# Kernel optimization log

Hardware: AMD Instinct MI355X
Metric: run time of the kernel (lower is better)

Reference implementation:

```python
import jax, jax.numpy as jnp
import numpy as np

N = 100_000          # nodes
E = 3_200_000        # train edges (avg degree 32)
E_TEST = 500_000     # pos/neg test edges each
F_IN, F_HID, F_OUT = 256, 16, 64


def setup_inputs() -> dict:
    key = jax.random.key(0)
    ks = jax.random.split(key, 7)
    x = jax.random.normal(ks[0], (N, F_IN), jnp.float32)
    train_edge_index = jax.random.randint(ks[1], (2, E), 0, N, dtype=jnp.int32)
    test_pos_edge_index = jax.random.randint(ks[2], (2, E_TEST), 0, N, dtype=jnp.int32)
    test_neg_edge_index = jax.random.randint(ks[3], (2, E_TEST), 0, N, dtype=jnp.int32)
    W1 = jax.random.normal(ks[4], (F_IN, F_HID), jnp.float32) / np.float32(np.sqrt(F_IN))
    b1 = jnp.zeros((F_HID,), jnp.float32)
    W2 = jax.random.normal(ks[5], (F_HID, F_OUT), jnp.float32) / np.float32(np.sqrt(F_HID))
    b2 = jnp.zeros((F_OUT,), jnp.float32)
    return dict(x=x, train_edge_index=train_edge_index,
                test_pos_edge_index=test_pos_edge_index,
                test_neg_edge_index=test_neg_edge_index,
                W1=W1, b1=b1, W2=W2, b2=b2)


def gcn_conv(x, edge_index, W, b, n):
    """PyG GCNConv: x' = D^-1/2 (A+I) D^-1/2 (x W) + b (self-loops added)."""
    h = x @ W                                  # project first (PyG order)
    loop = jnp.arange(n, dtype=edge_index.dtype)
    src = jnp.concatenate([edge_index[0], loop])
    dst = jnp.concatenate([edge_index[1], loop])
    deg = jax.ops.segment_sum(jnp.ones_like(dst, dtype=h.dtype), dst, num_segments=n)
    dinv = jnp.where(deg > 0, jax.lax.rsqrt(deg), 0.0)
    norm = dinv[src] * dinv[dst]               # per-edge symmetric norm
    msg = h[src] * norm[:, None]               # gather + scale
    out = jax.ops.segment_sum(msg, dst, num_segments=n)  # scatter-add
    return out + b


def reference(x, train_edge_index, test_pos_edge_index, test_neg_edge_index,
              W1, b1, W2, b2):
    n = x.shape[0]
    z = gcn_conv(x, train_edge_index, W1, b1, n)
    z = jax.nn.relu(z)
    z = gcn_conv(z, train_edge_index, W2, b2, n)
    edge_index = jnp.concatenate([test_pos_edge_index, test_neg_edge_index], axis=-1)
    logits = jnp.sum(z[edge_index[0]] * z[edge_index[1]], axis=-1)
    return logits
```

## Files before the change

### kernel.cpp

```cpp
#include <hip/hip_runtime.h>


#define NB_SHIFT 8
#define CAP   9728
#define CHUNK 8192

__global__ void seedprep_kernel(int* __restrict__ gtail, int nb1,
                                const float* __restrict__ W2, const float* __restrict__ b2,
                                float* __restrict__ mw) {
    int t = threadIdx.x;
    for (int i = t; i < nb1; i += 256) gtail[i] = i * CAP;
    int r = t >> 4, cc = t & 15;
    float s = 0.0f;
    for (int j = 0; j < 64; ++j) s += W2[r * 64 + j] * W2[cc * 64 + j];
    mw[t] = s;
    if (t < 16) {
        float w = 0.0f;
        for (int j = 0; j < 64; ++j) w += W2[t * 64 + j] * b2[j];
        mw[256 + t] = w;
    }
    if (t == 0) {
        float bbv = 0.0f;
        for (int j = 0; j < 64; ++j) bbv += b2[j] * b2[j];
        mw[272] = bbv;
    }
}

__global__ void __launch_bounds__(512, 4)
k1_kernel(const int* __restrict__ src, const int* __restrict__ dst, int E,
          int* __restrict__ gtail, unsigned* __restrict__ tmp, int nb1,
          const float* __restrict__ x, const float* __restrict__ W1,
          float* __restrict__ hs, int n, int nblkG) {
    int t = threadIdx.x;
    if ((int)blockIdx.x < nblkG) {
        int row = blockIdx.x * 512 + t;
        if (row >= n) return;
        const float4* x4 = (const float4*)(x + (size_t)row * 256);
        const float4* W14 = (const float4*)W1;
        float4 a0 = {0,0,0,0}, a1 = {0,0,0,0}, a2 = {0,0,0,0}, a3 = {0,0,0,0};
        float4 buf[8];
        #pragma unroll
        for (int j = 0; j < 8; ++j) buf[j] = x4[j];
        for (int k8 = 0; k8 < 8; ++k8) {
            float4 cur[8];
            #pragma unroll
            for (int j = 0; j < 8; ++j) cur[j] = buf[j];
            if (k8 < 7) {
                #pragma unroll
                for (int j = 0; j < 8; ++j) buf[j] = x4[(k8 + 1) * 8 + j];
            }
            #pragma unroll
            for (int jj = 0; jj < 8; ++jj) {
                float4 xv = cur[jj];
                int k4 = k8 * 8 + jj;
                #pragma unroll
                for (int j = 0; j < 4; ++j) {
                    float xk = (j == 0) ? xv.x : (j == 1) ? xv.y : (j == 2) ? xv.z : xv.w;
                    int k = (k4 << 2) + j;
                    float4 w0 = W14[k * 4 + 0];
                    float4 w1 = W14[k * 4 + 1];
                    float4 w2 = W14[k * 4 + 2];
                    float4 w3 = W14[k * 4 + 3];
                    a0.x += xk * w0.x; a0.y += xk * w0.y; a0.z += xk * w0.z; a0.w += xk * w0.w;
                    a1.x += xk * w1.x; a1.y += xk * w1.y; a1.z += xk * w1.z; a1.w += xk * w1.w;
                    a2.x += xk * w2.x; a2.y += xk * w2.y; a2.z += xk * w2.z; a2.w += xk * w2.w;
                    a3.x += xk * w3.x; a3.y += xk * w3.y; a3.z += xk * w3.z; a3.w += xk * w3.w;
                }
            }
        }
        float4* o = (float4*)(hs + (size_t)row * 16);
        o[0] = a0; o[1] = a1; o[2] = a2; o[3] = a3;
        return;
    }

    __shared__ int h[512];
    __shared__ int loff[512];
    __shared__ int cur[512];
    __shared__ int base[512];
    __shared__ unsigned srec[CHUNK];
    __shared__ unsigned short sbkt[CHUNK];
    int c0 = (blockIdx.x - nblkG) * CHUNK;
    int ce = min(CHUNK, E - c0);

    h[t] = 0;
    __syncthreads();
    for (int i = t; i < ce; i += 512)
        atomicAdd(&h[dst[c0 + i] >> NB_SHIFT], 1);
    __syncthreads();
    int cnt = h[t];
    loff[t] = cnt;
    __syncthreads();
    for (int off = 1; off < 512; off <<= 1) {
        int v = loff[t];
        int a = (t >= off) ? loff[t - off] : 0;
        __syncthreads();
        loff[t] = v + a;
        __syncthreads();
    }
    int excl = loff[t] - cnt;
    if (t < nb1) base[t] = atomicAdd(&gtail[t], cnt);
    loff[t] = excl;
    cur[t]  = excl;
    __syncthreads();
    for (int i = t; i < ce; i += 512) {
        int d = dst[c0 + i];
        int s = src[c0 + i];
        int b = d >> NB_SHIFT;
        int p = atomicAdd(&cur[b], 1);
        srec[p] = (unsigned)s | ((unsigned)(d & 255) << 20);
        sbkt[p] = (unsigned short)b;
    }
    __syncthreads();
    for (int i = t; i < ce; i += 512) {
        int b = sbkt[i];
        tmp[base[b] + (i - loff[b])] = srec[i];
    }
}

__global__ void __launch_bounds__(512)
fill2_kernel(const int* __restrict__ gtail, const unsigned* __restrict__ tmp,
             int* __restrict__ eidx, int* __restrict__ rowptr,
             int* __restrict__ counts, float* __restrict__ dinv,
             float* __restrict__ hs, int n) {
    __shared__ int hh[256];
    __shared__ int sc[256];
    __shared__ int cur[256];
    __shared__ float sdinv[256];
    __shared__ int sout[CAP];
    int b = blockIdx.x;
    int t = threadIdx.x;
    int beg = b * CAP;
    int cnt_total = gtail[b] - beg;

    if (t < 256) hh[t] = 0;
    __syncthreads();
    for (int i = t; i < cnt_total; i += 512)
        atomicAdd(&hh[tmp[beg + i] >> 20], 1);
    __syncthreads();
    if (t < 256) sc[t] = hh[t];
    __syncthreads();
    for (int off = 1; off < 256; off <<= 1) {
        int v = 0, a = 0;
        if (t < 256) { v = sc[t]; a = (t >= off) ? sc[t - off] : 0; }
        __syncthreads();
        if (t < 256) sc[t] = v + a;
        __syncthreads();
    }
    if (t < 256) {
        int ex = sc[t] - hh[t];
        cur[t] = ex;
        float dv = rsqrtf((float)hh[t] + 1.0f);
        sdinv[t] = dv;
        int v = (b << NB_SHIFT) + t;
        if (v < n) {
            rowptr[v] = beg + ex;
            counts[v] = hh[t];
            dinv[v]   = dv;
        }
    }
    __syncthreads();
    for (int i = t; i < cnt_total; i += 512) {
        unsigned r = tmp[beg + i];
        int p = atomicAdd(&cur[r >> 20], 1);
        sout[p] = (int)(r & 0xFFFFF);
    }
    __syncthreads();
    for (int i = t; i < cnt_total; i += 512)
        eidx[beg + i] = sout[i];
    int v0 = b << NB_SHIFT;
    int rows = min(256, n - v0);
    if (rows > 0) {
        float4* h4 = (float4*)(hs + (size_t)v0 * 16);
        int tot = rows * 4;
        for (int i = t; i < tot; i += 512) {
            float4 hv = h4[i];
            float dv = sdinv[i >> 2];
            hv.x *= dv; hv.y *= dv; hv.z *= dv; hv.w *= dv;
            h4[i] = hv;
        }
    }
}

__global__ void agg1_kernel(const int* __restrict__ rowptr, const int* __restrict__ counts,
                            const int* __restrict__ eidx, const float4* __restrict__ hs4,
                            const float* __restrict__ dinv, const float* __restrict__ b1,
                            float4* __restrict__ gs4, int n) {
    int t = blockIdx.x * blockDim.x + threadIdx.x;
    int v = t >> 3;
    if (v >= n) return;
    int q = t & 3, hh = (t >> 2) & 1;
    int start = rowptr[v], cnt = counts[v];
    float4 s = {0, 0, 0, 0};
    int i = hh;
    for (; i + 6 < cnt; i += 8) {
        int s0 = eidx[start + i];
        int s1 = eidx[start + i + 2];
        int s2 = eidx[start + i + 4];
        int s3 = eidx[start + i + 6];
        float4 h0 = hs4[(size_t)s0 * 4 + q];
        float4 h1 = hs4[(size_t)s1 * 4 + q];
        float4 h2 = hs4[(size_t)s2 * 4 + q];
        float4 h3 = hs4[(size_t)s3 * 4 + q];
        s.x += h0.x + h1.x + h2.x + h3.x;
        s.y += h0.y + h1.y + h2.y + h3.y;
        s.z += h0.z + h1.z + h2.z + h3.z;
        s.w += h0.w + h1.w + h2.w + h3.w;
    }
    for (; i < cnt; i += 2) {
        float4 h0 = hs4[(size_t)eidx[start + i] * 4 + q];
        s.x += h0.x; s.y += h0.y; s.z += h0.z; s.w += h0.w;
    }
    s.x += __shfl_xor(s.x, 4);
    s.y += __shfl_xor(s.y, 4);
    s.z += __shfl_xor(s.z, 4);
    s.w += __shfl_xor(s.w, 4);
    if (hh == 0) {
        float di = dinv[v];
        float4 h = hs4[(size_t)v * 4 + q];
        float4 b = ((const float4*)b1)[q];
        float4 z;
        z.x = fmaxf(di * (s.x + h.x) + b.x, 0.0f) * di;
        z.y = fmaxf(di * (s.y + h.y) + b.y, 0.0f) * di;
        z.z = fmaxf(di * (s.z + h.z) + b.z, 0.0f) * di;
        z.w = fmaxf(di * (s.w + h.w) + b.w, 0.0f) * di;
        gs4[(size_t)v * 4 + q] = z;
    }
}

__global__ void agg2y_kernel(const int* __restrict__ rowptr, const int* __restrict__ counts,
                             const int* __restrict__ eidx, const float4* __restrict__ gs4,
                             const float* __restrict__ dinv, const float* __restrict__ mw,
                             float4* __restrict__ u4, float* __restrict__ y,
                             float* __restrict__ c, int n) {
    __shared__ float su[32 * 16];
    __shared__ float sM[256];
    __shared__ float sw[16];
    int t = threadIdx.x;
    sM[t] = mw[t];
    if (t < 16) sw[t] = mw[256 + t];

    int j = t >> 3, q = t & 3, hh = (t >> 2) & 1;
    int v = blockIdx.x * 32 + j;
    if (v < n) {
        int start = rowptr[v], cnt = counts[v];
        float4 s = {0, 0, 0, 0};
        int i = hh;
        for (; i + 6 < cnt; i += 8) {
            int s0 = eidx[start + i];
            int s1 = eidx[start + i + 2];
            int s2 = eidx[start + i + 4];
            int s3 = eidx[start + i + 6];
            float4 g0 = gs4[(size_t)s0 * 4 + q];
            float4 g1 = gs4[(size_t)s1 * 4 + q];
            float4 g2 = gs4[(size_t)s2 * 4 + q];
            float4 g3 = gs4[(size_t)s3 * 4 + q];
            s.x += g0.x + g1.x + g2.x + g3.x;
            s.y += g0.y + g1.y + g2.y + g3.y;
            s.z += g0.z + g1.z + g2.z + g3.z;
            s.w += g0.w + g1.w + g2.w + g3.w;
        }
        for (; i < cnt; i += 2) {
            float4 g0 = gs4[(size_t)eidx[start + i] * 4 + q];
            s.x += g0.x; s.y += g0.y; s.z += g0.z; s.w += g0.w;
        }
        s.x += __shfl_xor(s.x, 4);
        s.y += __shfl_xor(s.y, 4);
        s.z += __shfl_xor(s.z, 4);
        s.w += __shfl_xor(s.w, 4);
        if (hh == 0) {
            float di = dinv[v];
            float4 g = gs4[(size_t)v * 4 + q];
            float4 uu;
            uu.x = di * (s.x + g.x);
            uu.y = di * (s.y + g.y);
            uu.z = di * (s.z + g.z);
            uu.w = di * (s.w + g.w);
            float* up = &su[j * 16 + q * 4];
            up[0] = uu.x; up[1] = uu.y; up[2] = uu.z; up[3] = uu.w;
            u4[(size_t)v * 4 + q] = uu;
        }
    }
    __syncthreads();
    if (v < n) {
        int l8 = t & 7;
        const float* uu = &su[j * 16];
        int c0 = l8 * 2;
        float y0 = sw[c0], y1 = sw[c0 + 1];
        #pragma unroll
        for (int k = 0; k < 16; ++k) {
            float uk = uu[k];
            y0 += uk * sM[k * 16 + c0];
            y1 += uk * sM[k * 16 + c0 + 1];
        }
        float2* yp = (float2*)(y + (size_t)v * 16 + c0);
        *yp = make_float2(y0, y1);
        if (l8 == 0) {
            float cv = 0.0f;
            #pragma unroll
            for (int k = 0; k < 16; ++k) cv += uu[k] * sw[k];
            c[v] = cv;
        }
    }
}

__global__ void edge_dot_kernel(const int* __restrict__ pa, const int* __restrict__ pb,
                                const int* __restrict__ na, const int* __restrict__ nb_,
                                int ET, const float* __restrict__ u, const float* __restrict__ y,
                                const float* __restrict__ c, const float* __restrict__ mw,
                                float* __restrict__ out) {
    int t = blockIdx.x * blockDim.x + threadIdx.x;
    int p = t >> 4, l = t & 15;
    if (p >= ET) return;
    int a0 = pa[p], b0 = pb[p];
    int a1 = na[p], b1 = nb_[p];
    float ya0 = y[(size_t)a0 * 16 + l];
    float ub0 = u[(size_t)b0 * 16 + l];
    float ya1 = y[(size_t)a1 * 16 + l];
    float ub1 = u[(size_t)b1 * 16 + l];
    float p0 = ya0 * ub0;
    float p1 = ya1 * ub1;
    p0 += __shfl_xor(p0, 1);  p1 += __shfl_xor(p1, 1);
    p0 += __shfl_xor(p0, 2);  p1 += __shfl_xor(p1, 2);
    p0 += __shfl_xor(p0, 4);  p1 += __shfl_xor(p1, 4);
    p0 += __shfl_xor(p0, 8);  p1 += __shfl_xor(p1, 8);
    if (l == 0) {
        float bb = mw[272];
        out[p]      = p0 + c[a0] + bb;
        out[ET + p] = p1 + c[a1] + bb;
    }
}

extern "C" void kernel_launch(void* const* d_in, const int* in_sizes, int n_in,
                              void* d_out, int out_size, void* d_ws, size_t ws_size,
                              hipStream_t stream) {
    const float* x    = (const float*)d_in[0];
    const int*   tei  = (const int*)d_in[1];
    const int*   tpos = (const int*)d_in[2];
    const int*   tneg = (const int*)d_in[3];
    const float* W1   = (const float*)d_in[4];
    const float* b1   = (const float*)d_in[5];
    const float* W2   = (const float*)d_in[6];
    const float* b2   = (const float*)d_in[7];
    float* out = (float*)d_out;

    int n   = in_sizes[0] / 256;
    int E   = in_sizes[1] / 2;
    int ET  = in_sizes[2] / 2;
    int nb1 = (n + 255) >> NB_SHIFT;

    char* w = (char*)d_ws;
    int*   gtail  = (int*)w;        w += 512 * 4;
    float* mw     = (float*)w;      w += 512 * 4;
    int*   rowptr = (int*)w;        w += (size_t)n * 4;
    int*   counts = (int*)w;        w += (size_t)n * 4;
    float* dinv   = (float*)w;      w += (size_t)n * 4;
    float* hs     = (float*)w;      w += (size_t)16 * n * 4;
    float* gs     = (float*)w;      w += (size_t)16 * n * 4;
    float* u      = (float*)w;      w += (size_t)16 * n * 4;
    float* y      = (float*)w;      w += (size_t)16 * n * 4;
    float* c      = (float*)w;      w += (size_t)n * 4;
    int*   eidx   = (int*)w;        w += (size_t)nb1 * CAP * 4;
    unsigned* tmp = (unsigned*)w;   w += (size_t)nb1 * CAP * 4;

    const int* src = tei;
    const int* dst = tei + E;

    int nblkA = (E + CHUNK - 1) / CHUNK;
    int nblkG = (n + 511) / 512;

    seedprep_kernel<<<1, 256, 0, stream>>>(gtail, nb1, W2, b2, mw);
    k1_kernel<<<nblkG + nblkA, 512, 0, stream>>>(src, dst, E, gtail, tmp, nb1,
                                                 x, W1, hs, n, nblkG);
    fill2_kernel<<<nb1, 512, 0, stream>>>(gtail, tmp, eidx, rowptr, counts, dinv, hs, n);

    agg1_kernel<<<(8 * n + 255) / 256, 256, 0, stream>>>(rowptr, counts, eidx,
                                                         (const float4*)hs, dinv, b1,
                                                         (float4*)gs, n);
    agg2y_kernel<<<(n + 31) / 32, 256, 0, stream>>>(rowptr, counts, eidx,
                                                    (const float4*)gs, dinv, mw,
                                                    (float4*)u, y, c, n);
    edge_dot_kernel<<<(16 * ET + 255) / 256, 256, 0, stream>>>(tpos, tpos + ET, tneg, tneg + ET,
                                                               ET, u, y, c, mw, out);
}
```

Baseline: 343.8 us.

## Split fused GEMM/bucketing kernel and stage x tiles through shared memory

The combined k1 kernel is split into a standalone X·W1 kernel and a separate edge-bucketing kernel, launched one after the other on the same stream. The GEMM now loads x cooperatively with coalesced float4 reads into a padded shared-memory tile and reads rows back from LDS, where before each thread streamed its own row with strided global loads. This targets the uncoalesced global traffic on the 100 MB x read. It costs an extra launch, loses the overlap between GEMM and bucketing blocks, and adds barriers plus LDS use in the GEMM.

```diff
diff --git a/kernel.cpp b/kernel.cpp
--- a/kernel.cpp
+++ b/kernel.cpp
@@ -26,60 +26,78 @@
     }
 }
 
-__global__ void __launch_bounds__(512, 4)
-k1_kernel(const int* __restrict__ src, const int* __restrict__ dst, int E,
-          int* __restrict__ gtail, unsigned* __restrict__ tmp, int nb1,
-          const float* __restrict__ x, const float* __restrict__ W1,
-          float* __restrict__ hs, int n, int nblkG) {
-    int t = threadIdx.x;
-    if ((int)blockIdx.x < nblkG) {
-        int row = blockIdx.x * 512 + t;
-        if (row >= n) return;
-        const float4* x4 = (const float4*)(x + (size_t)row * 256);
-        const float4* W14 = (const float4*)W1;
-        float4 a0 = {0,0,0,0}, a1 = {0,0,0,0}, a2 = {0,0,0,0}, a3 = {0,0,0,0};
-        float4 buf[8];
+__global__ void __launch_bounds__(256)
+gemm1_kernel(const float* __restrict__ x, const float* __restrict__ W1,
+             float* __restrict__ hs, int n) {
+    __shared__ float4 sx[256 * 9];
+    int t = threadIdx.x;
+    int rb = blockIdx.x << 8;
+    const float4* W14 = (const float4*)W1;
+    float4 a0 = {0,0,0,0}, a1 = {0,0,0,0}, a2 = {0,0,0,0}, a3 = {0,0,0,0};
+    float4 zero = {0,0,0,0};
+    float4 buf[8];
+    #pragma unroll
+    for (int j = 0; j < 8; ++j) {
+        int flat = t + (j << 8);
+        int r = flat >> 3, c = flat & 7;
+        int gr = rb + r;
+        buf[j] = (gr < n) ? ((const float4*)(x + (size_t)gr * 256))[c] : zero;
+    }
+    for (int ch = 0; ch < 8; ++ch) {
         #pragma unroll
-        for (int j = 0; j < 8; ++j) buf[j] = x4[j];
-        for (int k8 = 0; k8 < 8; ++k8) {
-            float4 cur[8];
+        for (int j = 0; j < 8; ++j) {
+            int flat = t + (j << 8);
+            sx[(flat >> 3) * 9 + (flat & 7)] = buf[j];
+        }
+        __syncthreads();
+        if (ch < 7) {
             #pragma unroll
-            for (int j = 0; j < 8; ++j) cur[j] = buf[j];
-            if (k8 < 7) {
-                #pragma unroll
-                for (int j = 0; j < 8; ++j) buf[j] = x4[(k8 + 1) * 8 + j];
+            for (int j = 0; j < 8; ++j) {
+                int flat = t + (j << 8);
+                int r = flat >> 3, c = flat & 7;
+                int gr = rb + r;
+                buf[j] = (gr < n)
+                    ? ((const float4*)(x + (size_t)gr * 256))[(ch + 1) * 8 + c] : zero;
             }
+        }
+        #pragma unroll
+        for (int c = 0; c < 8; ++c) {
+            float4 xv = sx[t * 9 + c];
+            int k4 = ch * 8 + c;
             #pragma unroll
-            for (int jj = 0; jj < 8; ++jj) {
-                float4 xv = cur[jj];
-                int k4 = k8 * 8 + jj;
-                #pragma unroll
-                for (int j = 0; j < 4; ++j) {
-                    float xk = (j == 0) ? xv.x : (j == 1) ? xv.y : (j == 2) ? xv.z : xv.w;
-                    int k = (k4 << 2) + j;
-                    float4 w0 = W14[k * 4 + 0];
-                    float4 w1 = W14[k * 4 + 1];
-                    float4 w2 = W14[k * 4 + 2];
-                    float4 w3 = W14[k * 4 + 3];
-                    a0.x += xk * w0.x; a0.y += xk * w0.y; a0.z += xk * w0.z; a0.w += xk * w0.w;
-                    a1.x += xk * w1.x; a1.y += xk * w1.y; a1.z += xk * w1.z; a1.w += xk * w1.w;
-                    a2.x += xk * w2.x; a2.y += xk * w2.y; a2.z += xk * w2.z; a2.w += xk * w2.w;
-                    a3.x += xk * w3.x; a3.y += xk * w3.y; a3.z += xk * w3.z; a3.w += xk * w3.w;
-                }
+            for (int j = 0; j < 4; ++j) {
+                float xk = (j == 0) ? xv.x : (j == 1) ? xv.y : (j == 2) ? xv.z : xv.w;
+                int k = (k4 << 2) + j;
+                float4 w0 = W14[k * 4 + 0];
+                float4 w1 = W14[k * 4 + 1];
+                float4 w2 = W14[k * 4 + 2];
+                float4 w3 = W14[k * 4 + 3];
+                a0.x += xk * w0.x; a0.y += xk * w0.y; a0.z += xk * w0.z; a0.w += xk * w0.w;
+                a1.x += xk * w1.x; a1.y += xk * w1.y; a1.z += xk * w1.z; a1.w += xk * w1.w;
+                a2.x += xk * w2.x; a2.y += xk * w2.y; a2.z += xk * w2.z; a2.w += xk * w2.w;
+                a3.x += xk * w3.x; a3.y += xk * w3.y; a3.z += xk * w3.z; a3.w += xk * w3.w;
             }
         }
+        __syncthreads();
+    }
+    int row = rb + t;
+    if (row < n) {
         float4* o = (float4*)(hs + (size_t)row * 16);
         o[0] = a0; o[1] = a1; o[2] = a2; o[3] = a3;
-        return;
-    }
-
+    }
+}
+
+__global__ void __launch_bounds__(512)
+passA1_kernel(const int* __restrict__ src, const int* __restrict__ dst, int E,
+              int* __restrict__ gtail, unsigned* __restrict__ tmp, int nb1) {
     __shared__ int h[512];
     __shared__ int loff[512];
     __shared__ int cur[512];
     __shared__ int base[512];
     __shared__ unsigned srec[CHUNK];
     __shared__ unsigned short sbkt[CHUNK];
-    int c0 = (blockIdx.x - nblkG) * CHUNK;
+    int t = threadIdx.x;
+    int c0 = blockIdx.x * CHUNK;
     int ce = min(CHUNK, E - c0);
 
     h[t] = 0;
@@ -365,12 +383,9 @@
     const int* src = tei;
     const int* dst = tei + E;
 
-    int nblkA = (E + CHUNK - 1) / CHUNK;
-    int nblkG = (n + 511) / 512;
-
     seedprep_kernel<<<1, 256, 0, stream>>>(gtail, nb1, W2, b2, mw);
-    k1_kernel<<<nblkG + nblkA, 512, 0, stream>>>(src, dst, E, gtail, tmp, nb1,
-                                                 x, W1, hs, n, nblkG);
+    gemm1_kernel<<<(n + 255) / 256, 256, 0, stream>>>(x, W1, hs, n);
+    passA1_kernel<<<(E + CHUNK - 1) / CHUNK, 512, 0, stream>>>(src, dst, E, gtail, tmp, nb1);
     fill2_kernel<<<nb1, 512, 0, stream>>>(gtail, tmp, eidx, rowptr, counts, dinv, hs, n);
 
     agg1_kernel<<<(8 * n + 255) / 256, 256, 0, stream>>>(rowptr, counts, eidx,
```

Result: slower. 367.4 us (+6.8%).
